# Kernel optimization log

Measured on AMD Instinct MI355X. Metric: run time of the kernel, lower is better.

## Reference

```python
import jax, jax.numpy as jnp
import numpy as np
import math

N = 32768
C = 128
K = 16
CHUNK = 2048
LN_EPS = float(C)  # original code calls torch.nn.LayerNorm(C, C): second positional arg is eps -> eps = 128.0 (faithful)


def knn_idx(coords):
    """Brute-force KNN on full coords [N,4] (matches knn_points(x_C, x_C, K=16)), chunked over queries."""
    def one_chunk(q):  # q: [CHUNK,4]
        d = jnp.sum((q[:, None, :] - coords[None, :, :]) ** 2, axis=-1)  # [CHUNK,N]
        return jax.lax.top_k(-d, K)[1]  # ascending distance (return_sorted=True)
    qs = coords.reshape(-1, CHUNK, coords.shape[-1])
    return jax.lax.map(one_chunk, qs).reshape(-1, K)  # [N,K]


def layer_norm(x, g, b):
    mu = jnp.mean(x, axis=-1, keepdims=True)
    var = jnp.mean((x - mu) ** 2, axis=-1, keepdims=True)
    return (x - mu) / jnp.sqrt(var + LN_EPS) * g + b


def self_attention(x_f, xyz_enc, new_feature, qw, qb, kw, kb, vw, vb):
    Q = x_f @ qw + qb                              # [N,C]
    nf = new_feature + xyz_enc                     # [N,K,C]
    Kt = nf @ kw + kb                              # [N,K,C]
    scores = jnp.einsum('nkd,nd->nk', Kt, Q) / math.sqrt(C)
    a = jax.nn.softmax(scores, axis=-1)            # [N,K]
    V = nf @ vw + vb                               # [N,K,C]
    return jnp.einsum('nk,nkd->nd', a, V)          # [N,C]


def setup_inputs() -> dict:
    key = jax.random.key(0)
    ks = jax.random.split(key, 22)
    xyz = jax.random.uniform(ks[0], (N, 3), dtype=jnp.float32) * 100.0
    coords = jnp.concatenate([jnp.zeros((N, 1), jnp.float32), xyz], axis=1)  # [N,4] batch col = 0
    feats = jax.random.normal(ks[1], (N, C), dtype=jnp.float32)
    s = 0.02
    def lin(k, din, dout):
        kw, kb = jax.random.split(k)
        return jax.random.normal(kw, (din, dout), jnp.float32) * s, jax.random.normal(kb, (dout,), jnp.float32) * s
    pos_w, pos_b = lin(ks[2], 3, C)
    pos1_w, pos1_b = lin(ks[3], 3, C)
    qw0, qb0 = lin(ks[4], C, C); kw0, kb0 = lin(ks[5], C, C); vw0, vb0 = lin(ks[6], C, C)
    qw1, qb1 = lin(ks[7], C, C); kw1, kb1 = lin(ks[8], C, C); vw1, vb1 = lin(ks[9], C, C)
    lin_w, lin_b = lin(ks[10], C, C)  # MinkowskiConvolution kernel_size=1 == pointwise linear
    return {
        'coords': coords, 'feats': feats,
        'pos_w': pos_w, 'pos_b': pos_b, 'pos1_w': pos1_w, 'pos1_b': pos1_b,
        'qw0': qw0, 'qb0': qb0, 'kw0': kw0, 'kb0': kb0, 'vw0': vw0, 'vb0': vb0,
        'qw1': qw1, 'qb1': qb1, 'kw1': kw1, 'kb1': kb1, 'vw1': vw1, 'vb1': vb1,
        'lin_w': lin_w, 'lin_b': lin_b,
        'g0': jnp.ones((C,), jnp.float32), 'be0': jnp.zeros((C,), jnp.float32),
        'g1': jnp.ones((C,), jnp.float32), 'be1': jnp.zeros((C,), jnp.float32),
    }


def reference(coords, feats, pos_w, pos_b, pos1_w, pos1_b,
              qw0, qb0, kw0, kb0, vw0, vb0,
              qw1, qb1, kw1, kb1, vw1, vb1,
              lin_w, lin_b, g0, be0, g1, be1):
    idx = knn_idx(coords)                           # [N,K]
    xyz = coords[:, 1:]                             # [N,3]
    new_xyz = xyz[:, None, :] - xyz[idx]            # [N,K,3] relative offsets
    # block 1
    xyz_enc = new_xyz @ pos_w + pos_b               # [N,K,C]
    nf = feats[idx]                                 # gather [N,K,C]
    o = self_attention(feats, xyz_enc, nf, qw0, qb0, kw0, kb0, vw0, vb0)
    # block 2: re-gather updated features with same idx
    nf1 = o[idx]
    xyz_enc1 = new_xyz @ pos1_w + pos1_b
    o = self_attention(o, xyz_enc1, nf1, qw1, qb1, kw1, kb1, vw1, vb1)
    # residual + LN, pointwise conv, residual + LN
    h = layer_norm(feats + o, g0, be0)
    h1 = h @ lin_w + lin_b
    return layer_norm(h + h1, g1, be1)
```

## Files before the change

### kernel.cpp

```cpp
#include <hip/hip_runtime.h>
#include <stdint.h>

#define NPT 32768

typedef unsigned int u32;
typedef unsigned short u16;
typedef unsigned long long u64;

typedef short v8s __attribute__((ext_vector_type(8)));
typedef float v4f __attribute__((ext_vector_type(4)));

__device__ __forceinline__ float b2f(u16 u) {
  union { u32 u; float f; } x; x.u = ((u32)u) << 16; return x.f;
}
__device__ __forceinline__ u16 f2b(float f) {
  union { float f; u32 u; } x; x.f = f;
  u32 u = x.u;
  return (u16)((u + 0x7fffu + ((u >> 16) & 1u)) >> 16);
}
__device__ __forceinline__ bool probe_f32(const void* coords) {
  return ((const u16*)coords)[1] == 0;
}
__device__ __forceinline__ float ldany(const void* p, long i, bool f32) {
  return f32 ? ((const float*)p)[i] : b2f(((const u16*)p)[i]);
}
__device__ __forceinline__ float wsum(float v) {
#pragma unroll
  for (int m = 1; m < 64; m <<= 1) v += __shfl_xor(v, m, 64);
  return v;
}
__device__ __forceinline__ v8s ldA8(const void* feats, long row, int off, bool f32) {
  union { uint4 u; v8s s; } c;
  if (f32) {
    const float* f = (const float*)feats + row * 128 + off;
    float4 x = *(const float4*)f;
    float4 y = *(const float4*)(f + 4);
    c.u.x = (u32)f2b(x.x) | ((u32)f2b(x.y) << 16);
    c.u.y = (u32)f2b(x.z) | ((u32)f2b(x.w) << 16);
    c.u.z = (u32)f2b(y.x) | ((u32)f2b(y.y) << 16);
    c.u.w = (u32)f2b(y.z) | ((u32)f2b(y.w) << 16);
  } else {
    c.u = *(const uint4*)((const u16*)feats + row * 128 + off);
  }
  return c.s;
}

#define GC 16
#define GH 6.25f
#define GINV 0.16f
#define NCELL (GC * GC * GC)

__device__ __forceinline__ int cell1d(float v) {
  int c = (int)(v * GINV);
  return c > (GC - 1) ? (GC - 1) : (c < 0 ? 0 : c);
}

__global__ __launch_bounds__(256) void conv_coords_hist(const void* __restrict__ coords,
                                                        float* __restrict__ cx, float* __restrict__ cy,
                                                        float* __restrict__ cz, int* __restrict__ cellStart,
                                                        int* __restrict__ pcell) {
  const bool f32 = probe_f32(coords);
  int i = blockIdx.x * 256 + threadIdx.x;
  float x = ldany(coords, (long)i * 4 + 1, f32);
  float y = ldany(coords, (long)i * 4 + 2, f32);
  float z = ldany(coords, (long)i * 4 + 3, f32);
  cx[i] = x; cy[i] = y; cz[i] = z;
  int c = (cell1d(z) * GC + cell1d(y)) * GC + cell1d(x);
  pcell[i] = c;
  atomicAdd(&cellStart[c + 1], 1);
}

__global__ __launch_bounds__(256) void grid_scan(int* __restrict__ cellStart, int* __restrict__ cellPtr) {
  __shared__ int part[256];
  const int t = threadIdx.x;
  int local[16]; int s = 0;
#pragma unroll
  for (int i = 0; i < 16; i++) { local[i] = cellStart[1 + t * 16 + i]; s += local[i]; }
  part[t] = s;
  __syncthreads();
  for (int off = 1; off < 256; off <<= 1) {
    int v = (t >= off) ? part[t - off] : 0;
    __syncthreads();
    part[t] += v;
    __syncthreads();
  }
  int run = (t == 0) ? 0 : part[t - 1];
#pragma unroll
  for (int i = 0; i < 16; i++) {
    int c = t * 16 + i;
    cellPtr[c] = run;
    run += local[i];
    cellStart[c + 1] = run;
  }
}

__global__ __launch_bounds__(256) void grid_scatter(const float* __restrict__ cx, const float* __restrict__ cy,
                                                    const float* __restrict__ cz, const int* __restrict__ pcell,
                                                    int* __restrict__ cellPtr, float4* __restrict__ sortedP,
                                                    int* __restrict__ rank) {
  int i = blockIdx.x * 256 + threadIdx.x;
  int c = pcell[i];
  int pos = atomicAdd(&cellPtr[c], 1);
  sortedP[pos] = make_float4(cx[i], cy[i], cz[i], __int_as_float(i));
  rank[i] = pos;
}

__device__ __forceinline__ void knn_body(int blk, int tid,
                                         const float4* __restrict__ sortedP,
                                         const int* __restrict__ cellStart,
                                         const int* __restrict__ rank,
                                         u16* __restrict__ idxout) {
  const int lane = tid & 63;
  const int gl = lane & 15;
  const int grp = lane >> 4;
  const int q = blk * 16 + (tid >> 4);
  const float4 p = sortedP[q];
  const float qx = p.x, qy = p.y, qz = p.z;
  const int qcx = cell1d(qx), qcy = cell1d(qy), qcz = cell1d(qz);
  const float fx = qx - qcx * GH, fy = qy - qcy * GH, fz = qz - qcz * GH;

  u64 R = ~0ull;

  auto key_of = [&](int g) -> u64 {
    float4 sp = sortedP[g];
    float dx = __fsub_rn(qx, sp.x), dy = __fsub_rn(qy, sp.y), dzc = __fsub_rn(qz, sp.z);
    float d = __fadd_rn(__fadd_rn(__fmul_rn(dx, dx), __fmul_rn(dy, dy)), __fmul_rn(dzc, dzc));
    return ((u64)__float_as_uint(d) << 32) | (u32)__float_as_int(sp.w);
  };

  auto shfl64 = [&](u64 v, int s) -> u64 {
    int lo = __shfl((int)(u32)v, s, 16);
    int hi = __shfl((int)(u32)(v >> 32), s, 16);
    return ((u64)(u32)hi << 32) | (u32)lo;
  };
  auto sxg = [&](u64 v, int m) -> u64 {
    int lo = __shfl_xor((int)(u32)v, m, 64);
    int hi = __shfl_xor((int)(u32)(v >> 32), m, 64);
    return ((u64)(u32)hi << 32) | (u32)lo;
  };
  auto upg = [&](u64 v) -> u64 {
    int lo = __shfl_up((int)(u32)v, 1, 16);
    int hi = __shfl_up((int)(u32)(v >> 32), 1, 16);
    return ((u64)(u32)hi << 32) | (u32)lo;
  };

  auto insert_one = [&](u64 kk) {
    u64 prev = upg(R);
    if (gl == 0) prev = 0ull;
    R = (kk < R) ? ((kk >= prev) ? kk : prev) : R;
  };

  auto batch_merge = [&](u64 key) {
    u64 k15 = shfl64(R, 15);
    u64 mask = __ballot(key < k15);
    u32 mymask = (u32)((mask >> (grp * 16)) & 0xffffu);
    if (mymask == 0) return;
    int pcount = __popc(mymask);
    if (pcount <= 8) {
      u32 mm = mymask;
      while (mm) {
        int s = __ffs((int)mm) - 1;
        mm &= mm - 1;
        insert_one(shfl64(key, s));
      }
      return;
    }
#pragma unroll
    for (int k = 2; k <= 16; k <<= 1) {
#pragma unroll
      for (int j = k >> 1; j > 0; j >>= 1) {
        u64 o = sxg(key, j);
        bool up = ((gl & k) == 0);
        bool lower = ((gl & j) == 0);
        u64 mn = key < o ? key : o;
        u64 mx = key < o ? o : key;
        key = (lower == up) ? mn : mx;
      }
    }
    u64 s = sxg(key, 15);
    u64 mn = R < s ? R : s;
#pragma unroll
    for (int j = 8; j > 0; j >>= 1) {
      u64 o = sxg(mn, j);
      bool lower = ((gl & j) == 0);
      u64 lo = mn < o ? mn : o;
      u64 hi = mn < o ? o : mn;
      mn = lower ? lo : hi;
    }
    R = mn;
  };

  auto scan_range_grp = [&](int s0, int s1) {
    if (s0 >= s1) return;
    int g0 = s0 + gl;
    u64 key = (g0 < s1) ? key_of(g0) : ~0ull;
    for (int base = s0; base < s1; base += 16) {
      int gn = base + 16 + gl;
      u64 nkey = (base + 16 < s1) ? ((gn < s1) ? key_of(gn) : ~0ull) : ~0ull;
      batch_merge(key);
      key = nkey;
    }
  };

  {
    const int xlo = qcx - 1 < 0 ? 0 : qcx - 1;
    const int xhi = qcx + 1 > GC - 1 ? GC - 1 : qcx + 1;
    {
      int rb = (qcz * GC + qcy) * GC;
      scan_range_grp(cellStart[rb + xlo], cellStart[rb + xhi + 1]);
    }
    const int rdz[8] = { 0, 0, -1, 1, -1, -1, 1, 1 };
    const int rdy[8] = { -1, 1, 0, 0, -1, 1, -1, 1 };
#pragma unroll
    for (int s_ = 0; s_ < 8; s_++) {
      int dz = rdz[s_], dy = rdy[s_];
      int z = qcz + dz, y = qcy + dy;
      if (z < 0 || z > GC - 1 || y < 0 || y > GC - 1) continue;
      float gz = (dz == 0) ? 0.f : (dz < 0 ? fz : GH - fz);
      float gy = (dy == 0) ? 0.f : (dy < 0 ? fy : GH - fy);
      float rowb = gz * gz + gy * gy;
      u64 k15 = shfl64(R, 15);
      float d15 = __uint_as_float((u32)(k15 >> 32));
      if (d15 < rowb * 0.998f - 1e-4f) continue;
      int rb = (z * GC + y) * GC;
      scan_range_grp(cellStart[rb + xlo], cellStart[rb + xhi + 1]);
    }
  }

  auto ubound = [&](int rr) -> float {
    float b = 1e30f;
    if (qcx - rr - 1 >= 0) b = fminf(b, fx + rr * GH);
    if (qcx + rr + 1 <= GC - 1) b = fminf(b, (rr + 1) * GH - fx);
    if (qcy - rr - 1 >= 0) b = fminf(b, fy + rr * GH);
    if (qcy + rr + 1 <= GC - 1) b = fminf(b, (rr + 1) * GH - fy);
    if (qcz - rr - 1 >= 0) b = fminf(b, fz + rr * GH);
    if (qcz + rr + 1 <= GC - 1) b = fminf(b, (rr + 1) * GH - fz);
    return b;
  };

  {
    u64 k15 = shfl64(R, 15);
    float d15 = __uint_as_float((u32)(k15 >> 32));
    float b1 = ubound(1);
    bool done = (b1 > 1e29f) || (d15 < b1 * b1 * 0.998f - 1e-4f);
    if (!done) {
      for (int r = 2; r < GC; ++r) {
        int zlo = qcz - r < 0 ? 0 : qcz - r, zhi = qcz + r > GC - 1 ? GC - 1 : qcz + r;
        for (int z = zlo; z <= zhi; ++z) {
          int adz = z - qcz; adz = adz < 0 ? -adz : adz;
          bool ez = (adz == r);
          int ylo = qcy - r < 0 ? 0 : qcy - r, yhi = qcy + r > GC - 1 ? GC - 1 : qcy + r;
          for (int y = ylo; y <= yhi; ++y) {
            int ady = y - qcy; ady = ady < 0 ? -ady : ady;
            bool ey = (ady == r);
            int rb = (z * GC + y) * GC;
            if (ez || ey) {
              int xlo = qcx - r < 0 ? 0 : qcx - r, xhi = qcx + r > GC - 1 ? GC - 1 : qcx + r;
              scan_range_grp(cellStart[rb + xlo], cellStart[rb + xhi + 1]);
            } else {
              int xm = qcx - r, xp = qcx + r;
              if (xm >= 0) scan_range_grp(cellStart[rb + xm], cellStart[rb + xm + 1]);
              if (xp <= GC - 1) scan_range_grp(cellStart[rb + xp], cellStart[rb + xp + 1]);
            }
          }
        }
        k15 = shfl64(R, 15);
        d15 = __uint_as_float((u32)(k15 >> 32));
        float b = ubound(r);
        if (b > 1e29f || d15 < b * b * 0.998f - 1e-4f) break;
      }
    }
  }

  idxout[(size_t)q * 16 + gl] = (u16)rank[(int)(u32)R];
}

__device__ __forceinline__ void gemm_body(int blk, int tid, const void* coords,
                                          const u16* __restrict__ A, const void* __restrict__ featsAny,
                                          const float4* __restrict__ sortedPtr,
                                          const u16* __restrict__ Bf, const void* __restrict__ bias,
                                          u16* __restrict__ Qb, u16* __restrict__ KVb,
                                          float* __restrict__ outF,
                                          const float* __restrict__ tblp, float* __restrict__ pOut,
                                          int mode, int ntiles) {
  const bool f32 = probe_f32(coords);
  const int lane = tid & 63;
  const int wave = tid >> 6;
  const int r0 = blk * 64 + wave * 16;
  const int quad = lane >> 4, lr = lane & 15;
  v8s a[4];
  if (sortedPtr) {
    long arow = (long)__float_as_int(sortedPtr[r0 + lr].w);
#pragma unroll
    for (int kq = 0; kq < 4; kq++) a[kq] = ldA8(featsAny, arow, kq * 32 + quad * 8, f32);
  } else {
#pragma unroll
    for (int kq = 0; kq < 4; kq++) {
      union { uint4 u; v8s s; } c;
      c.u = *(const uint4*)(A + (size_t)(r0 + lr) * 128 + kq * 32 + quad * 8);
      a[kq] = c.s;
    }
  }
  float pd0[4] = { 0.f, 0.f, 0.f, 0.f };
  float pd1[4] = { 0.f, 0.f, 0.f, 0.f };
  float pd2[4] = { 0.f, 0.f, 0.f, 0.f };
  float pd3[4] = { 0.f, 0.f, 0.f, 0.f };
  for (int tile = 0; tile < ntiles; ++tile) {
    v4f acc = { 0.f, 0.f, 0.f, 0.f };
#pragma unroll
    for (int kq = 0; kq < 4; kq++) {
      union { uint4 u; v8s s; } c;
      c.u = *(const uint4*)(Bf + ((size_t)(tile * 4 + kq) * 64 + lane) * 8);
      acc = __builtin_amdgcn_mfma_f32_16x16x32_bf16(a[kq], c.s, acc, 0, 0, 0);
    }
    int col = tile * 16 + lr;
    if (mode == 0) {
      if (col < 128) {
        float bb = ldany(bias, col, f32);
        float t0 = tblp[col], t1 = tblp[128 + col], t2 = tblp[256 + col], t3 = tblp[768 + col];
#pragma unroll
        for (int r = 0; r < 4; r++) {
          float qv = acc[r] + bb;
          Qb[(size_t)(r0 + quad * 4 + r) * 128 + col] = f2b(qv);
          pd0[r] += t0 * qv;
          pd1[r] += t1 * qv;
          pd2[r] += t2 * qv;
          pd3[r] += t3 * qv;
        }
      } else {
#pragma unroll
        for (int r = 0; r < 4; r++) KVb[(size_t)(r0 + quad * 4 + r) * 256 + (col - 128)] = f2b(acc[r]);
      }
    } else {
      float bb = ldany(bias, col, f32);
#pragma unroll
      for (int r = 0; r < 4; r++) outF[(size_t)(r0 + quad * 4 + r) * 128 + col] = acc[r] + bb;
    }
  }
  if (mode == 0) {
#pragma unroll
    for (int m = 1; m < 16; m <<= 1) {
#pragma unroll
      for (int r = 0; r < 4; r++) {
        pd0[r] += __shfl_xor(pd0[r], m, 64);
        pd1[r] += __shfl_xor(pd1[r], m, 64);
        pd2[r] += __shfl_xor(pd2[r], m, 64);
        pd3[r] += __shfl_xor(pd3[r], m, 64);
      }
    }
    if (lr < 4) {
#pragma unroll
      for (int r = 0; r < 4; r++) {
        float v = (lr == 0) ? pd0[r] : ((lr == 1) ? pd1[r] : ((lr == 2) ? pd2[r] : pd3[r]));
        pOut[(size_t)(r0 + quad * 4 + r) * 4 + lr] = v;
      }
    }
  }
}

__global__ __launch_bounds__(256) void knn_gemm0(const float4* __restrict__ sortedP,
                                                 const int* __restrict__ cellStart,
                                                 const int* __restrict__ rank,
                                                 u16* __restrict__ idxout,
                                                 const void* __restrict__ coords,
                                                 const void* __restrict__ feats,
                                                 const u16* __restrict__ Bf, const void* __restrict__ bias,
                                                 u16* __restrict__ Qb, u16* __restrict__ KVb,
                                                 const float* __restrict__ tblp, float* __restrict__ pOut) {
  if (blockIdx.x < 2048) {
    knn_body(blockIdx.x, threadIdx.x, sortedP, cellStart, rank, idxout);
  } else {
    gemm_body(blockIdx.x - 2048, threadIdx.x, coords, (const u16*)nullptr, feats, sortedP,
              Bf, bias, Qb, KVb, (float*)nullptr, tblp, pOut, 0, 24);
  }
}

__global__ __launch_bounds__(256) void gemm_kernel(const void* __restrict__ coords,
                                                   const u16* __restrict__ A, const u16* __restrict__ Bf,
                                                   const void* __restrict__ bias, u16* __restrict__ Qb,
                                                   u16* __restrict__ KVb, float* __restrict__ outF,
                                                   const float* __restrict__ tblp, float* __restrict__ pOut,
                                                   int mode, int ntiles) {
  gemm_body(blockIdx.x, threadIdx.x, coords, A, (const void*)nullptr, (const float4*)nullptr,
            Bf, bias, Qb, KVb, outF, tblp, pOut, mode, ntiles);
}

__global__ __launch_bounds__(256) void prep_tables(
    const void* coords,
    const void* pw0, const void* pb0, const void* kw0, const void* kb0, const void* vw0, const void* vb0,
    const void* pw1, const void* pb1, const void* kw1, const void* kb1, const void* vw1, const void* vb1,
    float* __restrict__ tbl, int* __restrict__ cellStart) {
  const bool f32 = probe_f32(coords);
  const int tid = blockIdx.x * 256 + threadIdx.x;
  if (tid <= NCELL) cellStart[tid] = 0;
  const int lane = threadIdx.x & 63;
  const int o = blockIdx.x * 4 + (threadIdx.x >> 6);
  const int l = o >> 10;
  const int rem = o & 1023;
  const void* PW = l ? pw1 : pw0;
  const void* PB = l ? pb1 : pb0;
  const void* KW = l ? kw1 : kw0;
  const void* KB = l ? kb1 : kb0;
  const void* VW = l ? vw1 : vw0;
  const void* VB = l ? vb1 : vb0;
  float acc, extra = 0.f;
  if (rem < 768) {
    bool isV = rem >= 384;
    int r2 = isV ? rem - 384 : rem;
    int i = r2 >> 7, c = r2 & 127;
    const void* W = isV ? VW : KW;
    acc = ldany(PW, i * 128 + lane, f32) * ldany(W, (long)lane * 128 + c, f32)
        + ldany(PW, i * 128 + lane + 64, f32) * ldany(W, (long)(lane + 64) * 128 + c, f32);
  } else {
    bool isV = rem >= 896;
    int c = rem & 127;
    const void* W = isV ? VW : KW;
    const void* B = isV ? VB : KB;
    acc = ldany(PB, lane, f32) * ldany(W, (long)lane * 128 + c, f32)
        + ldany(PB, lane + 64, f32) * ldany(W, (long)(lane + 64) * 128 + c, f32);
    extra = ldany(B, c, f32);
  }
  acc = wsum(acc) + extra;
  if (lane == 0) tbl[l * 1024 + rem] = acc;
}

__global__ __launch_bounds__(256) void prep_bfrag_all(const void* __restrict__ coords,
                                                      const void* __restrict__ qw0, const void* __restrict__ kw0,
                                                      const void* __restrict__ vw0, const void* __restrict__ qw1,
                                                      const void* __restrict__ kw1, const void* __restrict__ vw1,
                                                      const void* __restrict__ linw, u16* __restrict__ Bf0,
                                                      u16* __restrict__ Bf1, u16* __restrict__ BfL) {
  const bool f32 = probe_f32(coords);
  int tid = blockIdx.x * 256 + threadIdx.x;
  const void *w0, *w1, *w2; u16* out; int t;
  if (tid < 49152) { t = tid; w0 = qw0; w1 = kw0; w2 = vw0; out = Bf0; }
  else if (tid < 98304) { t = tid - 49152; w0 = qw1; w1 = kw1; w2 = vw1; out = Bf1; }
  else { t = tid - 98304; w0 = linw; w1 = linw; w2 = linw; out = BfL; }
  int j = t & 7, lane = (t >> 3) & 63, kq = (t >> 9) & 3, tile = t >> 11;
  int k = kq * 32 + ((lane >> 4) << 3) + j;
  int col = tile * 16 + (lane & 15);
  const void* w = (col < 128) ? w0 : ((col < 256) ? w1 : w2);
  long off = (long)k * 128 + (col & 127);
  out[t] = f32 ? f2b(((const float*)w)[off]) : ((const u16*)w)[off];
}

__global__ __launch_bounds__(256) void attn_kernel(const void* __restrict__ coordsRaw,
                                                   const float4* __restrict__ sortedP,
                                                   const u16* __restrict__ idx,
                                                   const u16* __restrict__ Qb, const u16* __restrict__ KVb,
                                                   const float* __restrict__ tbl, const float* __restrict__ p4,
                                                   const void* __restrict__ feats,
                                                   const void* __restrict__ g, const void* __restrict__ be,
                                                   u16* __restrict__ outB, int mode) {
  const int lane = threadIdx.x & 63;
  const int swz = (blockIdx.x & 7) * (gridDim.x >> 3) + (blockIdx.x >> 3);
  const int n = swz * 4 + (threadIdx.x >> 6);
  const int c0 = 2 * lane;
  const int k = lane & 15;
  const int quad = lane >> 4;
  const int base = lane & 48;

  const int j = idx[(size_t)n * 16 + k];
  u32 vr[16];
#pragma unroll
  for (int k2 = 0; k2 < 16; k2++) {
    int jk = __shfl(j, base + k2, 64);
    vr[k2] = *(const u32*)(KVb + (size_t)jk * 256 + 128 + c0);
  }
  uint4 kf[4];
#pragma unroll
  for (int kq = 0; kq < 4; kq++) {
    kf[kq] = *(const uint4*)(KVb + (size_t)j * 256 + kq * 32 + quad * 8);
  }
  const float4 P = sortedP[n];
  const float4 Pj = sortedP[j];
  const float nx = P.x - Pj.x, ny = P.y - Pj.y, nz = P.z - Pj.z;
  const float4 pv = *(const float4*)(p4 + (size_t)n * 4);

  v4f sacc = { 0.f, 0.f, 0.f, 0.f };
#pragma unroll
  for (int kq = 0; kq < 4; kq++) {
    union { uint4 u; v8s s; } ka, qa;
    ka.u = kf[kq];
    qa.u = *(const uint4*)(Qb + (size_t)n * 128 + kq * 32 + quad * 8);
    sacc = __builtin_amdgcn_mfma_f32_16x16x32_bf16(ka.s, qa.s, sacc, 0, 0, 0);
  }
  const int srcl = ((k >> 2) << 4) | k;
  float t0 = __shfl(sacc[0], srcl, 64);
  float t1 = __shfl(sacc[1], srcl, 64);
  float t2 = __shfl(sacc[2], srcl, 64);
  float t3 = __shfl(sacc[3], srcl, 64);
  float s = (k & 2) ? ((k & 1) ? t3 : t2) : ((k & 1) ? t1 : t0);
  float sc = (s + nx * pv.x + ny * pv.y + nz * pv.z + pv.w) * 0.08838834764831845f;

  float mx = sc;
#pragma unroll
  for (int m = 1; m < 16; m <<= 1) mx = fmaxf(mx, __shfl_xor(mx, m, 64));
  float e = expf(sc - mx);
  float ssum = e;
#pragma unroll
  for (int m = 1; m < 16; m <<= 1) ssum += __shfl_xor(ssum, m, 64);
  const float a = e / ssum;

  float wx = a * nx, wy = a * ny, wz = a * nz;
#pragma unroll
  for (int m = 1; m < 16; m <<= 1) {
    wx += __shfl_xor(wx, m, 64);
    wy += __shfl_xor(wy, m, 64);
    wz += __shfl_xor(wz, m, 64);
  }

  float a0 = 0.f, a1 = 0.f;
#pragma unroll
  for (int k2 = 0; k2 < 16; k2++) {
    float ak = __shfl(a, base + k2, 64);
    u32 u = vr[k2];
    a0 += ak * b2f((u16)(u & 0xffffu));
    a1 += ak * b2f((u16)(u >> 16));
  }
  float o0 = a0 + wx * tbl[384 + c0] + wy * tbl[512 + c0] + wz * tbl[640 + c0] + tbl[896 + c0];
  float o1 = a1 + wx * tbl[384 + c0 + 1] + wy * tbl[512 + c0 + 1] + wz * tbl[640 + c0 + 1] + tbl[896 + c0 + 1];
  if (mode == 1) {
    const bool f32 = probe_f32(coordsRaw);
    long orig = (long)__float_as_int(P.w);
    float x0 = ldany(feats, orig * 128 + c0, f32) + o0;
    float x1 = ldany(feats, orig * 128 + c0 + 1, f32) + o1;
    float mu = wsum(x0 + x1) * (1.f / 128.f);
    float d0 = x0 - mu, d1 = x1 - mu;
    float var = wsum(d0 * d0 + d1 * d1) * (1.f / 128.f);
    float rinv = 1.0f / sqrtf(var + 128.0f);
    o0 = d0 * rinv * ldany(g, c0, f32) + ldany(be, c0, f32);
    o1 = d1 * rinv * ldany(g, c0 + 1, f32) + ldany(be, c0 + 1, f32);
  }
  ((u32*)outB)[(size_t)n * 64 + lane] = (u32)f2b(o0) | ((u32)f2b(o1) << 16);
}

__global__ __launch_bounds__(256) void ln_final(const void* __restrict__ coords,
                                                const float4* __restrict__ sortedP,
                                                const u16* __restrict__ hB, const float* __restrict__ h1F,
                                                const void* __restrict__ g, const void* __restrict__ be,
                                                void* __restrict__ outAny) {
  const bool f32 = probe_f32(coords);
  const int lane = threadIdx.x & 63;
  const int n = blockIdx.x * 4 + (threadIdx.x >> 6);
  const int c0 = 2 * lane;
  u32 u = *(const u32*)(hB + (size_t)n * 128 + c0);
  float2 h1 = *(const float2*)(h1F + (size_t)n * 128 + c0);
  float x0 = b2f((u16)(u & 0xffffu)) + h1.x;
  float x1 = b2f((u16)(u >> 16)) + h1.y;
  float mu = wsum(x0 + x1) * (1.f / 128.f);
  float d0 = x0 - mu, d1 = x1 - mu;
  float var = wsum(d0 * d0 + d1 * d1) * (1.f / 128.f);
  float rinv = 1.0f / sqrtf(var + 128.0f);
  float y0 = d0 * rinv * ldany(g, c0, f32) + ldany(be, c0, f32);
  float y1 = d1 * rinv * ldany(g, c0 + 1, f32) + ldany(be, c0 + 1, f32);
  size_t orig = (size_t)__float_as_int(sortedP[n].w);
  if (f32) {
    *(float2*)((float*)outAny + orig * 128 + c0) = make_float2(y0, y1);
  } else {
    ((u32*)outAny)[orig * 64 + lane] = (u32)f2b(y0) | ((u32)f2b(y1) << 16);
  }
}

extern "C" void kernel_launch(void* const* d_in, const int* in_sizes, int n_in,
                              void* d_out, int out_size, void* d_ws, size_t ws_size,
                              hipStream_t stream) {
  (void)in_sizes; (void)n_in; (void)out_size; (void)ws_size;
  const void* coords = d_in[0];
  const void* feats = d_in[1];
  const void* pos_w = d_in[2];
  const void* pos_b = d_in[3];
  const void* pos1_w = d_in[4];
  const void* pos1_b = d_in[5];
  const void* qw0 = d_in[6];
  const void* qb0 = d_in[7];
  const void* kw0 = d_in[8];
  const void* kb0 = d_in[9];
  const void* vw0 = d_in[10];
  const void* vb0 = d_in[11];
  const void* qw1 = d_in[12];
  const void* qb1 = d_in[13];
  const void* kw1 = d_in[14];
  const void* kb1 = d_in[15];
  const void* vw1 = d_in[16];
  const void* vb1 = d_in[17];
  const void* lin_w = d_in[18];
  const void* lin_b = d_in[19];
  const void* g0 = d_in[20];
  const void* be0 = d_in[21];
  const void* g1 = d_in[22];
  const void* be1 = d_in[23];

  char* w = (char*)d_ws;
  u16* idxp = (u16*)(w + 0);
  float4* sortedP = (float4*)(w + 1048576);
  int* rank = (int*)(w + 1572864);
  float* cx = (float*)(w + 1703936);
  float* cy = (float*)(w + 1835008);
  float* cz = (float*)(w + 1966080);
  float* tbl = (float*)(w + 2097152);
  u16* Bf0 = (u16*)(w + 2105344);
  u16* Bf1 = (u16*)(w + 2203648);
  u16* BfL = (u16*)(w + 2301952);
  float* p4 = (float*)(w + 2334720);
  int* cellStart = (int*)(w + 2859008);
  int* cellPtr = (int*)(w + 2875456);
  int* pcell = (int*)(w + 2891840);
  u16* oS = (u16*)(w + 10723328);
  u16* Qb = (u16*)(w + 19111936);
  u16* KVb = (u16*)(w + 27500544);
  float* h1F = (float*)(w + 19111936);

  hipLaunchKernelGGL(prep_tables, dim3(512), dim3(256), 0, stream, coords,
                     pos_w, pos_b, kw0, kb0, vw0, vb0, pos1_w, pos1_b, kw1, kb1, vw1, vb1, tbl, cellStart);
  hipLaunchKernelGGL(conv_coords_hist, dim3(128), dim3(256), 0, stream, coords, cx, cy, cz, cellStart, pcell);
  hipLaunchKernelGGL(prep_bfrag_all, dim3(448), dim3(256), 0, stream, coords,
                     qw0, kw0, vw0, qw1, kw1, vw1, lin_w, Bf0, Bf1, BfL);

  hipLaunchKernelGGL(grid_scan, dim3(1), dim3(256), 0, stream, cellStart, cellPtr);
  hipLaunchKernelGGL(grid_scatter, dim3(128), dim3(256), 0, stream, cx, cy, cz, pcell, cellPtr, sortedP, rank);

  hipLaunchKernelGGL(knn_gemm0, dim3(2560), dim3(256), 0, stream, sortedP, cellStart, rank, idxp,
                     coords, feats, Bf0, qb0, Qb, KVb, tbl, p4);

  hipLaunchKernelGGL(attn_kernel, dim3(8192), dim3(256), 0, stream, coords, sortedP, idxp, Qb, KVb, tbl, p4,
                     (const void*)nullptr, (const void*)nullptr, (const void*)nullptr, oS, 0);
  hipLaunchKernelGGL(gemm_kernel, dim3(512), dim3(256), 0, stream, coords, oS, Bf1, qb1, Qb, KVb,
                     (float*)nullptr, tbl + 1024, p4, 0, 24);
  hipLaunchKernelGGL(attn_kernel, dim3(8192), dim3(256), 0, stream, coords, sortedP, idxp, Qb, KVb, tbl + 1024, p4,
                     feats, g0, be0, oS, 1);
  hipLaunchKernelGGL(gemm_kernel, dim3(512), dim3(256), 0, stream, coords, oS, BfL, lin_b,
                     (u16*)nullptr, (u16*)nullptr, h1F, (const float*)nullptr, (float*)nullptr, 1, 8);
  hipLaunchKernelGGL(ln_final, dim3(8192), dim3(256), 0, stream, coords, sortedP, oS, h1F, g1, be1, d_out);
}
```

Measured before the change: 296.6 us.

## Fuse final linear GEMM with residual LayerNorm and merge prep kernels

Replaces the final pointwise GEMM plus separate LayerNorm kernel with one gemm_ln kernel. It keeps the 128-column row in registers, adds the residual, and does the LayerNorm reduction with shuffles across the 16-lane groups. This drops the fp32 h1 round trip through memory and one launch. The three setup kernels (tables, coordinate histogram, B-fragment prep) become one prep_all launch, with the cellStart zeroing moved to hipMemsetAsync. The trade-off is that the final output stores become scattered 2-byte or 4-byte writes instead of vectorized ones.

```diff
diff --git a/kernel.cpp b/kernel.cpp
--- a/kernel.cpp
+++ b/kernel.cpp
@@ -53,21 +53,6 @@
 __device__ __forceinline__ int cell1d(float v) {
   int c = (int)(v * GINV);
   return c > (GC - 1) ? (GC - 1) : (c < 0 ? 0 : c);
-}
-
-__global__ __launch_bounds__(256) void conv_coords_hist(const void* __restrict__ coords,
-                                                        float* __restrict__ cx, float* __restrict__ cy,
-                                                        float* __restrict__ cz, int* __restrict__ cellStart,
-                                                        int* __restrict__ pcell) {
-  const bool f32 = probe_f32(coords);
-  int i = blockIdx.x * 256 + threadIdx.x;
-  float x = ldany(coords, (long)i * 4 + 1, f32);
-  float y = ldany(coords, (long)i * 4 + 2, f32);
-  float z = ldany(coords, (long)i * 4 + 3, f32);
-  cx[i] = x; cy[i] = y; cz[i] = z;
-  int c = (cell1d(z) * GC + cell1d(y)) * GC + cell1d(x);
-  pcell[i] = c;
-  atomicAdd(&cellStart[c + 1], 1);
 }
 
 __global__ __launch_bounds__(256) void grid_scan(int* __restrict__ cellStart, int* __restrict__ cellPtr) {
@@ -280,9 +265,8 @@
                                           const float4* __restrict__ sortedPtr,
                                           const u16* __restrict__ Bf, const void* __restrict__ bias,
                                           u16* __restrict__ Qb, u16* __restrict__ KVb,
-                                          float* __restrict__ outF,
                                           const float* __restrict__ tblp, float* __restrict__ pOut,
-                                          int mode, int ntiles) {
+                                          int ntiles) {
   const bool f32 = probe_f32(coords);
   const int lane = tid & 63;
   const int wave = tid >> 6;
@@ -314,30 +298,24 @@
       acc = __builtin_amdgcn_mfma_f32_16x16x32_bf16(a[kq], c.s, acc, 0, 0, 0);
     }
     int col = tile * 16 + lr;
-    if (mode == 0) {
-      if (col < 128) {
-        float bb = ldany(bias, col, f32);
-        float t0 = tblp[col], t1 = tblp[128 + col], t2 = tblp[256 + col], t3 = tblp[768 + col];
-#pragma unroll
-        for (int r = 0; r < 4; r++) {
-          float qv = acc[r] + bb;
-          Qb[(size_t)(r0 + quad * 4 + r) * 128 + col] = f2b(qv);
-          pd0[r] += t0 * qv;
-          pd1[r] += t1 * qv;
-          pd2[r] += t2 * qv;
-          pd3[r] += t3 * qv;
-        }
-      } else {
-#pragma unroll
-        for (int r = 0; r < 4; r++) KVb[(size_t)(r0 + quad * 4 + r) * 256 + (col - 128)] = f2b(acc[r]);
+    if (col < 128) {
+      float bb = ldany(bias, col, f32);
+      float t0 = tblp[col], t1 = tblp[128 + col], t2 = tblp[256 + col], t3 = tblp[768 + col];
+#pragma unroll
+      for (int r = 0; r < 4; r++) {
+        float qv = acc[r] + bb;
+        Qb[(size_t)(r0 + quad * 4 + r) * 128 + col] = f2b(qv);
+        pd0[r] += t0 * qv;
+        pd1[r] += t1 * qv;
+        pd2[r] += t2 * qv;
+        pd3[r] += t3 * qv;
       }
     } else {
-      float bb = ldany(bias, col, f32);
-#pragma unroll
-      for (int r = 0; r < 4; r++) outF[(size_t)(r0 + quad * 4 + r) * 128 + col] = acc[r] + bb;
-    }
-  }
-  if (mode == 0) {
+#pragma unroll
+      for (int r = 0; r < 4; r++) KVb[(size_t)(r0 + quad * 4 + r) * 256 + (col - 128)] = f2b(acc[r]);
+    }
+  }
+  {
 #pragma unroll
     for (int m = 1; m < 16; m <<= 1) {
 #pragma unroll
@@ -371,77 +349,166 @@
     knn_body(blockIdx.x, threadIdx.x, sortedP, cellStart, rank, idxout);
   } else {
     gemm_body(blockIdx.x - 2048, threadIdx.x, coords, (const u16*)nullptr, feats, sortedP,
-              Bf, bias, Qb, KVb, (float*)nullptr, tblp, pOut, 0, 24);
+              Bf, bias, Qb, KVb, tblp, pOut, 24);
   }
 }
 
 __global__ __launch_bounds__(256) void gemm_kernel(const void* __restrict__ coords,
                                                    const u16* __restrict__ A, const u16* __restrict__ Bf,
                                                    const void* __restrict__ bias, u16* __restrict__ Qb,
-                                                   u16* __restrict__ KVb, float* __restrict__ outF,
+                                                   u16* __restrict__ KVb,
                                                    const float* __restrict__ tblp, float* __restrict__ pOut,
-                                                   int mode, int ntiles) {
+                                                   int ntiles) {
   gemm_body(blockIdx.x, threadIdx.x, coords, A, (const void*)nullptr, (const float4*)nullptr,
-            Bf, bias, Qb, KVb, outF, tblp, pOut, mode, ntiles);
-}
-
-__global__ __launch_bounds__(256) void prep_tables(
+            Bf, bias, Qb, KVb, tblp, pOut, ntiles);
+}
+
+__global__ __launch_bounds__(256) void gemm_ln(const void* __restrict__ coords,
+                                               const u16* __restrict__ A ,
+                                               const u16* __restrict__ Bf, const void* __restrict__ bias,
+                                               const float4* __restrict__ sortedP,
+                                               const void* __restrict__ g, const void* __restrict__ be,
+                                               void* __restrict__ outAny) {
+  const bool f32 = probe_f32(coords);
+  const int lane = threadIdx.x & 63;
+  const int wave = threadIdx.x >> 6;
+  const int r0 = blockIdx.x * 64 + wave * 16;
+  const int quad = lane >> 4, lr = lane & 15;
+  v8s a[4];
+#pragma unroll
+  for (int kq = 0; kq < 4; kq++) {
+    union { uint4 u; v8s s; } c;
+    c.u = *(const uint4*)(A + (size_t)(r0 + lr) * 128 + kq * 32 + quad * 8);
+    a[kq] = c.s;
+  }
+  float xv[8][4];
+#pragma unroll
+  for (int tile = 0; tile < 8; ++tile) {
+    v4f acc = { 0.f, 0.f, 0.f, 0.f };
+#pragma unroll
+    for (int kq = 0; kq < 4; kq++) {
+      union { uint4 u; v8s s; } c;
+      c.u = *(const uint4*)(Bf + ((size_t)(tile * 4 + kq) * 64 + lane) * 8);
+      acc = __builtin_amdgcn_mfma_f32_16x16x32_bf16(a[kq], c.s, acc, 0, 0, 0);
+    }
+    int col = tile * 16 + lr;
+    float bb = ldany(bias, col, f32);
+#pragma unroll
+    for (int r = 0; r < 4; r++) {
+      float h = b2f(A[(size_t)(r0 + quad * 4 + r) * 128 + col]);
+      xv[tile][r] = h + acc[r] + bb;
+    }
+  }
+  float sum[4];
+#pragma unroll
+  for (int r = 0; r < 4; r++) {
+    sum[r] = 0.f;
+#pragma unroll
+    for (int tile = 0; tile < 8; ++tile) sum[r] += xv[tile][r];
+  }
+#pragma unroll
+  for (int m = 1; m < 16; m <<= 1) {
+#pragma unroll
+    for (int r = 0; r < 4; r++) sum[r] += __shfl_xor(sum[r], m, 64);
+  }
+  float mu[4];
+#pragma unroll
+  for (int r = 0; r < 4; r++) mu[r] = sum[r] * (1.f / 128.f);
+  float vs[4];
+#pragma unroll
+  for (int r = 0; r < 4; r++) {
+    vs[r] = 0.f;
+#pragma unroll
+    for (int tile = 0; tile < 8; ++tile) {
+      float d = xv[tile][r] - mu[r];
+      vs[r] += d * d;
+    }
+  }
+#pragma unroll
+  for (int m = 1; m < 16; m <<= 1) {
+#pragma unroll
+    for (int r = 0; r < 4; r++) vs[r] += __shfl_xor(vs[r], m, 64);
+  }
+  float rinv[4];
+#pragma unroll
+  for (int r = 0; r < 4; r++) rinv[r] = 1.0f / sqrtf(vs[r] * (1.f / 128.f) + 128.0f);
+  long orig[4];
+#pragma unroll
+  for (int r = 0; r < 4; r++) orig[r] = (long)__float_as_int(sortedP[r0 + quad * 4 + r].w);
+#pragma unroll
+  for (int tile = 0; tile < 8; ++tile) {
+    int col = tile * 16 + lr;
+    float gv = ldany(g, col, f32), bv = ldany(be, col, f32);
+#pragma unroll
+    for (int r = 0; r < 4; r++) {
+      float y = (xv[tile][r] - mu[r]) * rinv[r] * gv + bv;
+      if (f32) ((float*)outAny)[orig[r] * 128 + col] = y;
+      else ((u16*)outAny)[orig[r] * 128 + col] = f2b(y);
+    }
+  }
+}
+
+__global__ __launch_bounds__(256) void prep_all(
     const void* coords,
     const void* pw0, const void* pb0, const void* kw0, const void* kb0, const void* vw0, const void* vb0,
     const void* pw1, const void* pb1, const void* kw1, const void* kb1, const void* vw1, const void* vb1,
-    float* __restrict__ tbl, int* __restrict__ cellStart) {
+    float* __restrict__ tbl, int* __restrict__ cellStart,
+    float* __restrict__ cx, float* __restrict__ cy, float* __restrict__ cz, int* __restrict__ pcell,
+    const void* __restrict__ qw0, const void* __restrict__ qw1, const void* __restrict__ linw,
+    u16* __restrict__ Bf0, u16* __restrict__ Bf1, u16* __restrict__ BfL) {
   const bool f32 = probe_f32(coords);
-  const int tid = blockIdx.x * 256 + threadIdx.x;
-  if (tid <= NCELL) cellStart[tid] = 0;
-  const int lane = threadIdx.x & 63;
-  const int o = blockIdx.x * 4 + (threadIdx.x >> 6);
-  const int l = o >> 10;
-  const int rem = o & 1023;
-  const void* PW = l ? pw1 : pw0;
-  const void* PB = l ? pb1 : pb0;
-  const void* KW = l ? kw1 : kw0;
-  const void* KB = l ? kb1 : kb0;
-  const void* VW = l ? vw1 : vw0;
-  const void* VB = l ? vb1 : vb0;
-  float acc, extra = 0.f;
-  if (rem < 768) {
-    bool isV = rem >= 384;
-    int r2 = isV ? rem - 384 : rem;
-    int i = r2 >> 7, c = r2 & 127;
-    const void* W = isV ? VW : KW;
-    acc = ldany(PW, i * 128 + lane, f32) * ldany(W, (long)lane * 128 + c, f32)
-        + ldany(PW, i * 128 + lane + 64, f32) * ldany(W, (long)(lane + 64) * 128 + c, f32);
+  if (blockIdx.x < 512) {
+    const int lane = threadIdx.x & 63;
+    const int o = blockIdx.x * 4 + (threadIdx.x >> 6);
+    const int l = o >> 10;
+    const int rem = o & 1023;
+    const void* PW = l ? pw1 : pw0;
+    const void* PB = l ? pb1 : pb0;
+    const void* KW = l ? kw1 : kw0;
+    const void* KB = l ? kb1 : kb0;
+    const void* VW = l ? vw1 : vw0;
+    const void* VB = l ? vb1 : vb0;
+    float acc, extra = 0.f;
+    if (rem < 768) {
+      bool isV = rem >= 384;
+      int r2 = isV ? rem - 384 : rem;
+      int i = r2 >> 7, c = r2 & 127;
+      const void* W = isV ? VW : KW;
+      acc = ldany(PW, i * 128 + lane, f32) * ldany(W, (long)lane * 128 + c, f32)
+          + ldany(PW, i * 128 + lane + 64, f32) * ldany(W, (long)(lane + 64) * 128 + c, f32);
+    } else {
+      bool isV = rem >= 896;
+      int c = rem & 127;
+      const void* W = isV ? VW : KW;
+      const void* B = isV ? VB : KB;
+      acc = ldany(PB, lane, f32) * ldany(W, (long)lane * 128 + c, f32)
+          + ldany(PB, lane + 64, f32) * ldany(W, (long)(lane + 64) * 128 + c, f32);
+      extra = ldany(B, c, f32);
+    }
+    acc = wsum(acc) + extra;
+    if (lane == 0) tbl[l * 1024 + rem] = acc;
+  } else if (blockIdx.x < 640) {
+    int i = (blockIdx.x - 512) * 256 + threadIdx.x;
+    float x = ldany(coords, (long)i * 4 + 1, f32);
+    float y = ldany(coords, (long)i * 4 + 2, f32);
+    float z = ldany(coords, (long)i * 4 + 3, f32);
+    cx[i] = x; cy[i] = y; cz[i] = z;
+    int c = (cell1d(z) * GC + cell1d(y)) * GC + cell1d(x);
+    pcell[i] = c;
+    atomicAdd(&cellStart[c + 1], 1);
   } else {
-    bool isV = rem >= 896;
-    int c = rem & 127;
-    const void* W = isV ? VW : KW;
-    const void* B = isV ? VB : KB;
-    acc = ldany(PB, lane, f32) * ldany(W, (long)lane * 128 + c, f32)
-        + ldany(PB, lane + 64, f32) * ldany(W, (long)(lane + 64) * 128 + c, f32);
-    extra = ldany(B, c, f32);
-  }
-  acc = wsum(acc) + extra;
-  if (lane == 0) tbl[l * 1024 + rem] = acc;
-}
-
-__global__ __launch_bounds__(256) void prep_bfrag_all(const void* __restrict__ coords,
-                                                      const void* __restrict__ qw0, const void* __restrict__ kw0,
-                                                      const void* __restrict__ vw0, const void* __restrict__ qw1,
-                                                      const void* __restrict__ kw1, const void* __restrict__ vw1,
-                                                      const void* __restrict__ linw, u16* __restrict__ Bf0,
-                                                      u16* __restrict__ Bf1, u16* __restrict__ BfL) {
-  const bool f32 = probe_f32(coords);
-  int tid = blockIdx.x * 256 + threadIdx.x;
-  const void *w0, *w1, *w2; u16* out; int t;
-  if (tid < 49152) { t = tid; w0 = qw0; w1 = kw0; w2 = vw0; out = Bf0; }
-  else if (tid < 98304) { t = tid - 49152; w0 = qw1; w1 = kw1; w2 = vw1; out = Bf1; }
-  else { t = tid - 98304; w0 = linw; w1 = linw; w2 = linw; out = BfL; }
-  int j = t & 7, lane = (t >> 3) & 63, kq = (t >> 9) & 3, tile = t >> 11;
-  int k = kq * 32 + ((lane >> 4) << 3) + j;
-  int col = tile * 16 + (lane & 15);
-  const void* w = (col < 128) ? w0 : ((col < 256) ? w1 : w2);
-  long off = (long)k * 128 + (col & 127);
-  out[t] = f32 ? f2b(((const float*)w)[off]) : ((const u16*)w)[off];
+    int tid = (blockIdx.x - 640) * 256 + threadIdx.x;
+    const void *w0, *w1, *w2; u16* out; int t;
+    if (tid < 49152) { t = tid; w0 = qw0; w1 = kw0; w2 = vw0; out = Bf0; }
+    else if (tid < 98304) { t = tid - 49152; w0 = qw1; w1 = kw1; w2 = vw1; out = Bf1; }
+    else { t = tid - 98304; w0 = linw; w1 = linw; w2 = linw; out = BfL; }
+    int j = t & 7, lane = (t >> 3) & 63, kq = (t >> 9) & 3, tile = t >> 11;
+    int k = kq * 32 + ((lane >> 4) << 3) + j;
+    int col = tile * 16 + (lane & 15);
+    const void* w = (col < 128) ? w0 : ((col < 256) ? w1 : w2);
+    long off = (long)k * 128 + (col & 127);
+    out[t] = f32 ? f2b(((const float*)w)[off]) : ((const u16*)w)[off];
+  }
 }
 
 __global__ __launch_bounds__(256) void attn_kernel(const void* __restrict__ coordsRaw,
@@ -533,33 +600,6 @@
     o1 = d1 * rinv * ldany(g, c0 + 1, f32) + ldany(be, c0 + 1, f32);
   }
   ((u32*)outB)[(size_t)n * 64 + lane] = (u32)f2b(o0) | ((u32)f2b(o1) << 16);
-}
-
-__global__ __launch_bounds__(256) void ln_final(const void* __restrict__ coords,
-                                                const float4* __restrict__ sortedP,
-                                                const u16* __restrict__ hB, const float* __restrict__ h1F,
-                                                const void* __restrict__ g, const void* __restrict__ be,
-                                                void* __restrict__ outAny) {
-  const bool f32 = probe_f32(coords);
-  const int lane = threadIdx.x & 63;
-  const int n = blockIdx.x * 4 + (threadIdx.x >> 6);
-  const int c0 = 2 * lane;
-  u32 u = *(const u32*)(hB + (size_t)n * 128 + c0);
-  float2 h1 = *(const float2*)(h1F + (size_t)n * 128 + c0);
-  float x0 = b2f((u16)(u & 0xffffu)) + h1.x;
-  float x1 = b2f((u16)(u >> 16)) + h1.y;
-  float mu = wsum(x0 + x1) * (1.f / 128.f);
-  float d0 = x0 - mu, d1 = x1 - mu;
-  float var = wsum(d0 * d0 + d1 * d1) * (1.f / 128.f);
-  float rinv = 1.0f / sqrtf(var + 128.0f);
-  float y0 = d0 * rinv * ldany(g, c0, f32) + ldany(be, c0, f32);
-  float y1 = d1 * rinv * ldany(g, c0 + 1, f32) + ldany(be, c0 + 1, f32);
-  size_t orig = (size_t)__float_as_int(sortedP[n].w);
-  if (f32) {
-    *(float2*)((float*)outAny + orig * 128 + c0) = make_float2(y0, y1);
-  } else {
-    ((u32*)outAny)[orig * 64 + lane] = (u32)f2b(y0) | ((u32)f2b(y1) << 16);
-  }
 }
 
 extern "C" void kernel_launch(void* const* d_in, const int* in_sizes, int n_in,
@@ -609,13 +649,12 @@
   u16* oS = (u16*)(w + 10723328);
   u16* Qb = (u16*)(w + 19111936);
   u16* KVb = (u16*)(w + 27500544);
-  float* h1F = (float*)(w + 19111936);
-
-  hipLaunchKernelGGL(prep_tables, dim3(512), dim3(256), 0, stream, coords,
-                     pos_w, pos_b, kw0, kb0, vw0, vb0, pos1_w, pos1_b, kw1, kb1, vw1, vb1, tbl, cellStart);
-  hipLaunchKernelGGL(conv_coords_hist, dim3(128), dim3(256), 0, stream, coords, cx, cy, cz, cellStart, pcell);
-  hipLaunchKernelGGL(prep_bfrag_all, dim3(448), dim3(256), 0, stream, coords,
-                     qw0, kw0, vw0, qw1, kw1, vw1, lin_w, Bf0, Bf1, BfL);
+
+  hipMemsetAsync(cellStart, 0, (NCELL + 1) * sizeof(int), stream);
+
+  hipLaunchKernelGGL(prep_all, dim3(1088), dim3(256), 0, stream, coords,
+                     pos_w, pos_b, kw0, kb0, vw0, vb0, pos1_w, pos1_b, kw1, kb1, vw1, vb1,
+                     tbl, cellStart, cx, cy, cz, pcell, qw0, qw1, lin_w, Bf0, Bf1, BfL);
 
   hipLaunchKernelGGL(grid_scan, dim3(1), dim3(256), 0, stream, cellStart, cellPtr);
   hipLaunchKernelGGL(grid_scatter, dim3(128), dim3(256), 0, stream, cx, cy, cz, pcell, cellPtr, sortedP, rank);
@@ -626,10 +665,8 @@
   hipLaunchKernelGGL(attn_kernel, dim3(8192), dim3(256), 0, stream, coords, sortedP, idxp, Qb, KVb, tbl, p4,
                      (const void*)nullptr, (const void*)nullptr, (const void*)nullptr, oS, 0);
   hipLaunchKernelGGL(gemm_kernel, dim3(512), dim3(256), 0, stream, coords, oS, Bf1, qb1, Qb, KVb,
-                     (float*)nullptr, tbl + 1024, p4, 0, 24);
+                     tbl + 1024, p4, 24);
   hipLaunchKernelGGL(attn_kernel, dim3(8192), dim3(256), 0, stream, coords, sortedP, idxp, Qb, KVb, tbl + 1024, p4,
                      feats, g0, be0, oS, 1);
-  hipLaunchKernelGGL(gemm_kernel, dim3(512), dim3(256), 0, stream, coords, oS, BfL, lin_b,
-                     (u16*)nullptr, (u16*)nullptr, h1F, (const float*)nullptr, (float*)nullptr, 1, 8);
-  hipLaunchKernelGGL(ln_final, dim3(8192), dim3(256), 0, stream, coords, sortedP, oS, h1F, g1, be1, d_out);
-}
+  hipLaunchKernelGGL(gemm_ln, dim3(512), dim3(256), 0, stream, coords, oS, BfL, lin_b, sortedP, g1, be1, d_out);
+}
```

After: 285.9 us. 1.04x faster.
